# Kernel tuning notes

Measured on AMD Instinct MI355X. Metric: run time of the kernel, lower is better.

Reference implementation:

```python
import jax, jax.numpy as jnp
import numpy as np

EPS = 1e-6  # flax.linen.LayerNorm default epsilon
ETA_BASE = 1.0

def _ln(h, g, b):
    m = jnp.mean(h, axis=-1, keepdims=True)
    v = jnp.var(h, axis=-1, keepdims=True)
    return (h - m) * jax.lax.rsqrt(v + EPS) * g + b

def setup_inputs() -> dict:
    key = jax.random.key(0)
    ks = jax.random.split(key, 8)
    B, D, H = 8192, 2048, 64
    sD = 1.0 / np.sqrt(D).astype(np.float32)
    sH = 1.0 / np.sqrt(H).astype(np.float32)
    return {
        "x": jax.random.normal(ks[0], (B, D), jnp.float32),
        "Wk": jax.random.normal(ks[1], (D, H), jnp.float32) * sD,
        "bk": jnp.zeros((H,), jnp.float32),
        "Wv": jax.random.normal(ks[2], (D, H), jnp.float32) * sD,
        "bv": jnp.zeros((H,), jnp.float32),
        "Wq": jax.random.normal(ks[3], (D, H), jnp.float32) * sD,
        "bq": jnp.zeros((H,), jnp.float32),
        "Wo": jax.random.normal(ks[4], (H, D), jnp.float32) * sH,
        "bo": jnp.zeros((D,), jnp.float32),
        "ln_g": jnp.ones((H,), jnp.float32),
        "ln_b": jnp.zeros((H,), jnp.float32),
        "w_lr": jax.random.normal(ks[5], (D, 1), jnp.float32) * sD,
        "b_lr": jnp.zeros((1,), jnp.float32),
        "W_init": jax.random.normal(ks[6], (H, H), jnp.float32) * 0.01,
    }

def reference(x, Wk, bk, Wv, bv, Wq, bq, Wo, bo, ln_g, ln_b, w_lr, b_lr, W_init):
    # One TTT adaptation step per token (vmapped over the batch of tokens),
    # each starting from the shared learnable initial state W_init.
    def step(xi):  # xi: (D,)
        k = xi @ Wk + bk                      # (H,) training view
        v = xi @ Wv + bv                      # (H,) label view
        def loss_fn(W):
            pred = k + _ln(k @ W.T, ln_g, ln_b)   # f(k; W) = k + LN(Wk)
            return jnp.mean((pred - v) ** 2)
        ssl_loss, grad_W = jax.value_and_grad(loss_fn)(W_init)
        eta = ETA_BASE * jax.nn.sigmoid(xi @ w_lr + b_lr)[0]
        W_new = W_init - eta * grad_W         # (H, H) inner-loop SGD step
        q = xi @ Wq + bq                      # (H,) output view
        z = (q + _ln(q @ W_new.T, ln_g, ln_b)) @ Wo + bo  # (D,)
        return z, W_new, ssl_loss
    z, W_new, ssl_loss = jax.vmap(step)(x)
    return z, W_new, ssl_loss
```

## Files before the change

### kernel.cpp

```cpp
#include <hip/hip_runtime.h>
#include <cstdint>
#include <cstddef>
#include <math.h>

#define D_DIM 2048
#define H_DIM 64
#define B_TOK 8192
#define NCAT  256

__global__ __launch_bounds__(256) void pack_w(const float* __restrict__ Wk,
                                              const float* __restrict__ Wv,
                                              const float* __restrict__ Wq,
                                              const float* __restrict__ wlr,
                                              float* __restrict__ Wcat) {
    int idx = blockIdx.x * 256 + threadIdx.x;
    int d = idx >> 8, n = idx & 255;
    float val;
    if (n < 64)        val = Wk[d * 64 + n];
    else if (n < 128)  val = Wv[d * 64 + (n - 64)];
    else if (n < 192)  val = Wq[d * 64 + (n - 128)];
    else if (n == 192) val = wlr[d];
    else               val = 0.0f;
    Wcat[idx] = val;
}

__global__ __launch_bounds__(256) void gemm1(const float* __restrict__ x,
                                             const float* __restrict__ Wcat,
                                             float* __restrict__ C) {
    __shared__ float As[32][64];
    __shared__ float Bs[32][64];
    const int m0 = blockIdx.x * 64;
    const int n0 = blockIdx.y * 64;
    const int tid = threadIdx.x;
    const int tx = tid & 15, ty = tid >> 4;

    const int arow = tid >> 2;
    const int acol = (tid & 3) * 8;
    const int bkr  = tid >> 4;
    const int bcol = (tid & 15) * 4;

    float acc[4][4] = {};

    for (int k0 = 0; k0 < D_DIM; k0 += 32) {
        float4 a0 = *(const float4*)(x + (size_t)(m0 + arow) * D_DIM + k0 + acol);
        float4 a1 = *(const float4*)(x + (size_t)(m0 + arow) * D_DIM + k0 + acol + 4);
        float4 b0 = *(const float4*)(Wcat + (size_t)(k0 + bkr)      * NCAT + n0 + bcol);
        float4 b1 = *(const float4*)(Wcat + (size_t)(k0 + bkr + 16) * NCAT + n0 + bcol);
        As[acol + 0][arow] = a0.x; As[acol + 1][arow] = a0.y;
        As[acol + 2][arow] = a0.z; As[acol + 3][arow] = a0.w;
        As[acol + 4][arow] = a1.x; As[acol + 5][arow] = a1.y;
        As[acol + 6][arow] = a1.z; As[acol + 7][arow] = a1.w;
        *(float4*)&Bs[bkr][bcol]      = b0;
        *(float4*)&Bs[bkr + 16][bcol] = b1;
        __syncthreads();
        #pragma unroll
        for (int k = 0; k < 32; ++k) {
            float4 a = *(const float4*)&As[k][ty * 4];
            float4 b = *(const float4*)&Bs[k][tx * 4];
            float ar[4] = {a.x, a.y, a.z, a.w};
            float br[4] = {b.x, b.y, b.z, b.w};
            #pragma unroll
            for (int i = 0; i < 4; ++i)
                #pragma unroll
                for (int j = 0; j < 4; ++j)
                    acc[i][j] = fmaf(ar[i], br[j], acc[i][j]);
        }
        __syncthreads();
    }
    #pragma unroll
    for (int i = 0; i < 4; ++i) {
        float4 o = make_float4(acc[i][0], acc[i][1], acc[i][2], acc[i][3]);
        *(float4*)(C + (size_t)(m0 + ty * 4 + i) * NCAT + n0 + tx * 4) = o;
    }
}

__device__ __forceinline__ float wsum64(float x) {
    #pragma unroll
    for (int o = 32; o > 0; o >>= 1) x += __shfl_xor(x, o, 64);
    return x;
}

__global__ __launch_bounds__(256) void ttt_step(
    const float* __restrict__ C, const float* __restrict__ W_init,
    const float* __restrict__ bk_, const float* __restrict__ bv_,
    const float* __restrict__ bq_, const float* __restrict__ blr_,
    const float* __restrict__ ln_g, const float* __restrict__ ln_b,
    float* __restrict__ Wnew_out, float* __restrict__ ssl_out,
    float* __restrict__ u_out) {
    __shared__ float Wi[64][65];
    __shared__ float sk[4][64], sq[4][64], sdh[4][64];
    const int tid = threadIdx.x;
    const int w = tid >> 6, lane = tid & 63;

    for (int i = tid; i < 4096; i += 256)
        Wi[i >> 6][i & 63] = W_init[i];

    const int t = blockIdx.x * 4 + w;
    const float* Ct = C + (size_t)t * NCAT;
    float k = Ct[lane] + bk_[lane];
    float v = Ct[64 + lane] + bv_[lane];
    float q = Ct[128 + lane] + bq_[lane];
    float elog = Ct[192] + blr_[0];
    float eta = 1.0f / (1.0f + expf(-elog));

    sk[w][lane] = k;
    sq[w][lane] = q;
    __syncthreads();

    float h = 0.0f, hq = 0.0f;
    #pragma unroll
    for (int j = 0; j < 64; ++j) {
        float wj = Wi[lane][j];
        h  = fmaf(wj, sk[w][j], h);
        hq = fmaf(wj, sq[w][j], hq);
    }

    const float g = ln_g[lane], bb = ln_b[lane];
    float m1  = wsum64(h) * (1.0f / 64.0f);
    float hc  = h - m1;
    float var1 = wsum64(hc * hc) * (1.0f / 64.0f);
    float rs1 = rsqrtf(var1 + 1e-6f);
    float hhat = hc * rs1;
    float pred = k + hhat * g + bb;
    float diff = pred - v;
    float ssl = wsum64(diff * diff) * (1.0f / 64.0f);
    float dhhat = (2.0f / 64.0f) * diff * g;
    float s1 = wsum64(dhhat) * (1.0f / 64.0f);
    float s2 = wsum64(dhhat * hhat) * (1.0f / 64.0f);
    float dh = rs1 * (dhhat - s1 - hhat * s2);
    sdh[w][lane] = dh;

    float kq = wsum64(k * q);
    float wq = hq - eta * kq * dh;
    float m2 = wsum64(wq) * (1.0f / 64.0f);
    float wc = wq - m2;
    float var2 = wsum64(wc * wc) * (1.0f / 64.0f);
    float rs2 = rsqrtf(var2 + 1e-6f);
    float u = q + wc * rs2 * g + bb;
    u_out[(size_t)t * 64 + lane] = u;
    if (lane == 0) ssl_out[t] = ssl;

    float* Wout = Wnew_out + (size_t)t * 4096;
    const int r_off = lane >> 4;
    const int c4 = (lane & 15) * 4;
    #pragma unroll
    for (int rr = 0; rr < 16; ++rr) {
        int r = rr * 4 + r_off;
        float e = eta * sdh[w][r];
        float4 o;
        o.x = Wi[r][c4 + 0] - e * sk[w][c4 + 0];
        o.y = Wi[r][c4 + 1] - e * sk[w][c4 + 1];
        o.z = Wi[r][c4 + 2] - e * sk[w][c4 + 2];
        o.w = Wi[r][c4 + 3] - e * sk[w][c4 + 3];
        *(float4*)(Wout + r * 64 + c4) = o;
    }
}

__global__ __launch_bounds__(256) void gemm2(const float* __restrict__ u,
                                             const float* __restrict__ Wo,
                                             const float* __restrict__ bo,
                                             float* __restrict__ z) {
    __shared__ float Ut[64][64];
    __shared__ float Ws[64][64];
    const int m0 = blockIdx.x * 64;
    const int n0 = blockIdx.y * 64;
    const int tid = threadIdx.x;
    const int tx = tid & 15, ty = tid >> 4;

    {
        int row = tid >> 2, c0 = (tid & 3) * 16;
        const float4* src = (const float4*)(u + (size_t)(m0 + row) * 64 + c0);
        #pragma unroll
        for (int f = 0; f < 4; ++f) {
            float4 a = src[f];
            Ut[c0 + f * 4 + 0][row] = a.x;
            Ut[c0 + f * 4 + 1][row] = a.y;
            Ut[c0 + f * 4 + 2][row] = a.z;
            Ut[c0 + f * 4 + 3][row] = a.w;
        }
        int kr = tid >> 2;
        const float4* wsrc = (const float4*)(Wo + (size_t)kr * D_DIM + n0 + c0);
        #pragma unroll
        for (int f = 0; f < 4; ++f)
            *(float4*)&Ws[kr][c0 + f * 4] = wsrc[f];
    }
    __syncthreads();

    float acc[4][4] = {};
    #pragma unroll
    for (int k = 0; k < 64; ++k) {
        float4 a = *(const float4*)&Ut[k][ty * 4];
        float4 b = *(const float4*)&Ws[k][tx * 4];
        float ar[4] = {a.x, a.y, a.z, a.w};
        float br[4] = {b.x, b.y, b.z, b.w};
        #pragma unroll
        for (int i = 0; i < 4; ++i)
            #pragma unroll
            for (int j = 0; j < 4; ++j)
                acc[i][j] = fmaf(ar[i], br[j], acc[i][j]);
    }
    float4 bo4 = *(const float4*)(bo + n0 + tx * 4);
    #pragma unroll
    for (int i = 0; i < 4; ++i) {
        float4 o = make_float4(acc[i][0] + bo4.x, acc[i][1] + bo4.y,
                               acc[i][2] + bo4.z, acc[i][3] + bo4.w);
        *(float4*)(z + (size_t)(m0 + ty * 4 + i) * D_DIM + n0 + tx * 4) = o;
    }
}

extern "C" void kernel_launch(void* const* d_in, const int* in_sizes, int n_in,
                              void* d_out, int out_size, void* d_ws, size_t ws_size,
                              hipStream_t stream) {
    const float* x    = (const float*)d_in[0];
    const float* Wk   = (const float*)d_in[1];
    const float* bk   = (const float*)d_in[2];
    const float* Wv   = (const float*)d_in[3];
    const float* bv   = (const float*)d_in[4];
    const float* Wq   = (const float*)d_in[5];
    const float* bq   = (const float*)d_in[6];
    const float* Wo   = (const float*)d_in[7];
    const float* bo   = (const float*)d_in[8];
    const float* ln_g = (const float*)d_in[9];
    const float* ln_b = (const float*)d_in[10];
    const float* wlr  = (const float*)d_in[11];
    const float* blr  = (const float*)d_in[12];
    const float* Wini = (const float*)d_in[13];

    float* z_out   = (float*)d_out;
    float* Wn_out  = z_out + (size_t)B_TOK * D_DIM;
    float* ssl_out = Wn_out + (size_t)B_TOK * H_DIM * H_DIM;

    float* Wcat = (float*)d_ws;
    float* C    = Wcat + (size_t)D_DIM * NCAT;
    float* u    = C + (size_t)B_TOK * NCAT;

    pack_w<<<D_DIM, 256, 0, stream>>>(Wk, Wv, Wq, wlr, Wcat);
    gemm1<<<dim3(B_TOK / 64, NCAT / 64), 256, 0, stream>>>(x, Wcat, C);
    ttt_step<<<B_TOK / 4, 256, 0, stream>>>(C, Wini, bk, bv, bq, blr,
                                            ln_g, ln_b, Wn_out, ssl_out, u);
    gemm2<<<dim3(B_TOK / 64, D_DIM / 64), 256, 0, stream>>>(u, Wo, bo, z_out);
}
```

Baseline: 398.3 us.

## Rewrite first projection GEMM on bf16 MFMA with split-precision hi/lo emulation

Replaces the FP32 SIMT tiled GEMM for the fused K/V/Q/lr projection with a matrix-core kernel using bf16 MFMA 16x16x32. FP32 accuracy is approximated by splitting each operand into high and low bf16 parts and doing three MFMA products. The packing kernel now pre-splits the weights into hi/lo bf16 in a k-blocked layout, and the GEMM double-buffers B in shared memory and register-prefetches A. It trades extra conversion work and a small precision loss for much higher matrix throughput on the x·Wcat GEMM (8192x2048x256).

Result: faster. 345.7 us (-13.2%).

```diff
diff --git a/kernel.cpp b/kernel.cpp
--- a/kernel.cpp
+++ b/kernel.cpp
@@ -8,69 +8,141 @@
 #define B_TOK 8192
 #define NCAT  256
 
-__global__ __launch_bounds__(256) void pack_w(const float* __restrict__ Wk,
-                                              const float* __restrict__ Wv,
-                                              const float* __restrict__ Wq,
-                                              const float* __restrict__ wlr,
-                                              float* __restrict__ Wcat) {
-    int idx = blockIdx.x * 256 + threadIdx.x;
-    int d = idx >> 8, n = idx & 255;
-    float val;
-    if (n < 64)        val = Wk[d * 64 + n];
-    else if (n < 128)  val = Wv[d * 64 + (n - 64)];
-    else if (n < 192)  val = Wq[d * 64 + (n - 128)];
-    else if (n == 192) val = wlr[d];
-    else               val = 0.0f;
-    Wcat[idx] = val;
-}
-
-__global__ __launch_bounds__(256) void gemm1(const float* __restrict__ x,
-                                             const float* __restrict__ Wcat,
-                                             float* __restrict__ C) {
-    __shared__ float As[32][64];
-    __shared__ float Bs[32][64];
+typedef short s16x8 __attribute__((ext_vector_type(8)));
+typedef float f32x4 __attribute__((ext_vector_type(4)));
+
+__global__ __launch_bounds__(256) void pack_w2(const float* __restrict__ Wk,
+                                               const float* __restrict__ Wv,
+                                               const float* __restrict__ Wq,
+                                               const float* __restrict__ wlr,
+                                               uint4* __restrict__ Wh,
+                                               uint4* __restrict__ Wl) {
+    int id = blockIdx.x * 256 + threadIdx.x;
+    int Gd = id >> 8, n = id & 255;
+    unsigned short hb[8], lb[8];
+    #pragma unroll
+    for (int j = 0; j < 8; ++j) {
+        int d = Gd * 8 + j;
+        float val;
+        if (n < 64)        val = Wk[d * 64 + n];
+        else if (n < 128)  val = Wv[d * 64 + (n - 64)];
+        else if (n < 192)  val = Wq[d * 64 + (n - 128)];
+        else if (n == 192) val = wlr[d];
+        else               val = 0.0f;
+        unsigned int xb = __float_as_uint(val);
+        hb[j] = (unsigned short)(xb >> 16);
+        float hf = __uint_as_float(xb & 0xFFFF0000u);
+        lb[j] = (unsigned short)(__float_as_uint(val - hf) >> 16);
+    }
+    uint4 oh, ol;
+    oh.x = hb[0] | ((unsigned int)hb[1] << 16);
+    oh.y = hb[2] | ((unsigned int)hb[3] << 16);
+    oh.z = hb[4] | ((unsigned int)hb[5] << 16);
+    oh.w = hb[6] | ((unsigned int)hb[7] << 16);
+    ol.x = lb[0] | ((unsigned int)lb[1] << 16);
+    ol.y = lb[2] | ((unsigned int)lb[3] << 16);
+    ol.z = lb[4] | ((unsigned int)lb[5] << 16);
+    ol.w = lb[6] | ((unsigned int)lb[7] << 16);
+    Wh[id] = oh;
+    Wl[id] = ol;
+}
+
+__device__ __forceinline__ void cvt_hl(const float4& a, const float4& b,
+                                       s16x8& h, s16x8& l) {
+    float v[8] = {a.x, a.y, a.z, a.w, b.x, b.y, b.z, b.w};
+    #pragma unroll
+    for (int j = 0; j < 8; ++j) {
+        unsigned int xb = __float_as_uint(v[j]);
+        h[j] = (short)(xb >> 16);
+        float hf = __uint_as_float(xb & 0xFFFF0000u);
+        l[j] = (short)(__float_as_uint(v[j] - hf) >> 16);
+    }
+}
+
+#define MFMA __builtin_amdgcn_mfma_f32_16x16x32_bf16
+
+#define GBODY(K, CUR, NXT, BP0, BP1, BN0, BN1, AP0, AP1, AP2, AP3, AN0, AN1, AN2, AN3) \
+  { \
+    const s16x8* BHp = (const s16x8*)&Bh[CUR][0]; \
+    const s16x8* BLp = (const s16x8*)&Bl[CUR][0]; \
+    s16x8 bh0 = BHp[bgi], bh1 = BHp[bgi + 16]; \
+    s16x8 bl0 = BLp[bgi], bl1 = BLp[bgi + 16]; \
+    Bh[NXT][tid] = BP0; Bl[NXT][tid] = BP1; \
+    int kb2 = (((K) + 2 <= 63) ? (K) + 2 : 63) * 4; \
+    BN0 = Wh[kb2 * 256 + srcoff]; \
+    BN1 = Wl[kb2 * 256 + srcoff]; \
+    int ka = (((K) + 1 <= 63) ? (K) + 1 : 63) * 32; \
+    AN0 = *(const float4*)(ax0 + ka);     AN1 = *(const float4*)(ax0 + ka + 4); \
+    AN2 = *(const float4*)(ax1 + ka);     AN3 = *(const float4*)(ax1 + ka + 4); \
+    s16x8 ah0, al0, ah1, al1; \
+    cvt_hl(AP0, AP1, ah0, al0); \
+    cvt_hl(AP2, AP3, ah1, al1); \
+    acc00 = MFMA(ah0, bh0, acc00, 0, 0, 0); \
+    acc01 = MFMA(ah0, bh1, acc01, 0, 0, 0); \
+    acc10 = MFMA(ah1, bh0, acc10, 0, 0, 0); \
+    acc11 = MFMA(ah1, bh1, acc11, 0, 0, 0); \
+    acc00 = MFMA(ah0, bl0, acc00, 0, 0, 0); \
+    acc01 = MFMA(ah0, bl1, acc01, 0, 0, 0); \
+    acc10 = MFMA(ah1, bl0, acc10, 0, 0, 0); \
+    acc11 = MFMA(ah1, bl1, acc11, 0, 0, 0); \
+    acc00 = MFMA(al0, bh0, acc00, 0, 0, 0); \
+    acc01 = MFMA(al0, bh1, acc01, 0, 0, 0); \
+    acc10 = MFMA(al1, bh0, acc10, 0, 0, 0); \
+    acc11 = MFMA(al1, bh1, acc11, 0, 0, 0); \
+    __syncthreads(); \
+  }
+
+__global__ __launch_bounds__(256) void gemm1m(const float* __restrict__ x,
+                                              const uint4* __restrict__ Wh,
+                                              const uint4* __restrict__ Wl,
+                                              float* __restrict__ C) {
+    __shared__ uint4 Bh[2][256];
+    __shared__ uint4 Bl[2][256];
+    const int tid  = threadIdx.x;
+    const int lane = tid & 63;
+    const int wave = tid >> 6;
+    const int wm = wave >> 1, wn = wave & 1;
+    const int l15 = lane & 15, l4 = lane >> 4;
     const int m0 = blockIdx.x * 64;
     const int n0 = blockIdx.y * 64;
-    const int tid = threadIdx.x;
-    const int tx = tid & 15, ty = tid >> 4;
-
-    const int arow = tid >> 2;
-    const int acol = (tid & 3) * 8;
-    const int bkr  = tid >> 4;
-    const int bcol = (tid & 15) * 4;
-
-    float acc[4][4] = {};
-
-    for (int k0 = 0; k0 < D_DIM; k0 += 32) {
-        float4 a0 = *(const float4*)(x + (size_t)(m0 + arow) * D_DIM + k0 + acol);
-        float4 a1 = *(const float4*)(x + (size_t)(m0 + arow) * D_DIM + k0 + acol + 4);
-        float4 b0 = *(const float4*)(Wcat + (size_t)(k0 + bkr)      * NCAT + n0 + bcol);
-        float4 b1 = *(const float4*)(Wcat + (size_t)(k0 + bkr + 16) * NCAT + n0 + bcol);
-        As[acol + 0][arow] = a0.x; As[acol + 1][arow] = a0.y;
-        As[acol + 2][arow] = a0.z; As[acol + 3][arow] = a0.w;
-        As[acol + 4][arow] = a1.x; As[acol + 5][arow] = a1.y;
-        As[acol + 6][arow] = a1.z; As[acol + 7][arow] = a1.w;
-        *(float4*)&Bs[bkr][bcol]      = b0;
-        *(float4*)&Bs[bkr + 16][bcol] = b1;
-        __syncthreads();
-        #pragma unroll
-        for (int k = 0; k < 32; ++k) {
-            float4 a = *(const float4*)&As[k][ty * 4];
-            float4 b = *(const float4*)&Bs[k][tx * 4];
-            float ar[4] = {a.x, a.y, a.z, a.w};
-            float br[4] = {b.x, b.y, b.z, b.w};
-            #pragma unroll
-            for (int i = 0; i < 4; ++i)
-                #pragma unroll
-                for (int j = 0; j < 4; ++j)
-                    acc[i][j] = fmaf(ar[i], br[j], acc[i][j]);
-        }
-        __syncthreads();
-    }
-    #pragma unroll
-    for (int i = 0; i < 4; ++i) {
-        float4 o = make_float4(acc[i][0], acc[i][1], acc[i][2], acc[i][3]);
-        *(float4*)(C + (size_t)(m0 + ty * 4 + i) * NCAT + n0 + tx * 4) = o;
+
+    const float* ax0 = x + (size_t)(m0 + wm * 32 + l15) * D_DIM + l4 * 8;
+    const float* ax1 = ax0 + (size_t)16 * D_DIM;
+    const int srcoff = (tid >> 6) * 256 + n0 + (tid & 63);
+    const int bgi = l4 * 64 + wn * 32 + l15;
+
+    f32x4 z4 = {0.f, 0.f, 0.f, 0.f};
+    f32x4 acc00 = z4, acc01 = z4, acc10 = z4, acc11 = z4;
+
+    {
+        uint4 t0 = Wh[srcoff], t1 = Wl[srcoff];
+        Bh[0][tid] = t0; Bl[0][tid] = t1;
+    }
+    float4 apA0 = *(const float4*)(ax0);
+    float4 apA1 = *(const float4*)(ax0 + 4);
+    float4 apA2 = *(const float4*)(ax1);
+    float4 apA3 = *(const float4*)(ax1 + 4);
+    uint4 bpA0 = Wh[4 * 256 + srcoff];
+    uint4 bpA1 = Wl[4 * 256 + srcoff];
+    float4 apB0, apB1, apB2, apB3;
+    uint4  bpB0, bpB1;
+    __syncthreads();
+
+    #pragma unroll 1
+    for (int k = 0; k < 64; k += 2) {
+        GBODY(k,     0, 1, bpA0, bpA1, bpB0, bpB1,
+              apA0, apA1, apA2, apA3, apB0, apB1, apB2, apB3)
+        GBODY(k + 1, 1, 0, bpB0, bpB1, bpA0, bpA1,
+              apB0, apB1, apB2, apB3, apA0, apA1, apA2, apA3)
+    }
+
+    float* cp = C + (size_t)(m0 + wm * 32 + l4 * 4) * NCAT + n0 + wn * 32 + l15;
+    #pragma unroll
+    for (int r = 0; r < 4; ++r) {
+        cp[(size_t)r * NCAT +  0]        = acc00[r];
+        cp[(size_t)r * NCAT + 16]        = acc01[r];
+        cp[(size_t)(16 + r) * NCAT +  0] = acc10[r];
+        cp[(size_t)(16 + r) * NCAT + 16] = acc11[r];
     }
 }
 
@@ -230,12 +302,13 @@
     float* Wn_out  = z_out + (size_t)B_TOK * D_DIM;
     float* ssl_out = Wn_out + (size_t)B_TOK * H_DIM * H_DIM;
 
-    float* Wcat = (float*)d_ws;
-    float* C    = Wcat + (size_t)D_DIM * NCAT;
-    float* u    = C + (size_t)B_TOK * NCAT;
-
-    pack_w<<<D_DIM, 256, 0, stream>>>(Wk, Wv, Wq, wlr, Wcat);
-    gemm1<<<dim3(B_TOK / 64, NCAT / 64), 256, 0, stream>>>(x, Wcat, C);
+    uint4* Wh = (uint4*)d_ws;
+    uint4* Wl = Wh + 65536;
+    float* C  = (float*)(Wl + 65536);
+    float* u  = C + (size_t)B_TOK * NCAT;
+
+    pack_w2<<<256, 256, 0, stream>>>(Wk, Wv, Wq, wlr, Wh, Wl);
+    gemm1m<<<dim3(B_TOK / 64, NCAT / 64), 256, 0, stream>>>(x, Wh, Wl, C);
     ttt_step<<<B_TOK / 4, 256, 0, stream>>>(C, Wini, bk, bv, bq, blr,
                                             ln_g, ln_b, Wn_out, ssl_out, u);
     gemm2<<<dim3(B_TOK / 64, D_DIM / 64), 256, 0, stream>>>(u, Wo, bo, z_out);
```
